# Optimization experiments

Measured on AMD Instinct MI355X. Metric: run time of the kernel, lower is better.

The kernel has to match this reference:

```python
import jax, jax.numpy as jnp
import numpy as np
from jax import lax

EPS = 1e-5
DW_TH = 4.0   # threshold in cut_conv3_5_DW
PW_TH = 1e-3  # threshold in cut_conv3_5_PW


def _bn(x, gamma, beta, mean, var):
    # inference-mode batchnorm over channel dim (NCHW)
    scale = (gamma * lax.rsqrt(var + EPS))[None, :, None, None]
    shift = (beta - mean * gamma * lax.rsqrt(var + EPS))[None, :, None, None]
    return x * scale + shift


def _channel_cut(x, th):
    # faithful to max(torch.max(x[m][k]), -torch.min(x[m][k])) == max |x| per (n, c)
    max_obs = jnp.max(jnp.abs(x), axis=(2, 3), keepdims=True)  # [N, C, 1, 1]
    return jnp.where(max_obs < th, jnp.zeros_like(x), x)


def setup_inputs() -> dict:
    key = jax.random.key(0)
    ks = jax.random.split(key, 6)
    N, Cin, Cout, H, W = 32, 256, 512, 56, 56
    x = jax.random.normal(ks[0], (N, Cin, H, W), dtype=jnp.float32)
    dw_w = jax.random.normal(ks[1], (Cin, 1, 3, 3), dtype=jnp.float32) * 0.3
    dw_b = jax.random.normal(ks[2], (Cin,), dtype=jnp.float32) * 0.1
    pw_w = jax.random.normal(ks[3], (Cout, Cin), dtype=jnp.float32) * 0.05
    pw_b = jax.random.normal(ks[4], (Cout,), dtype=jnp.float32) * 0.1
    return {
        "x": x,
        "dw_w": dw_w,
        "dw_b": dw_b,
        "bn1_gamma": jnp.ones((Cin,), jnp.float32) * 2.0,
        "bn1_beta": jnp.zeros((Cin,), jnp.float32),
        "bn1_mean": jnp.zeros((Cin,), jnp.float32),
        "bn1_var": jnp.ones((Cin,), jnp.float32),
        "pw_w": pw_w,
        "pw_b": pw_b,
        "bn2_gamma": jnp.ones((Cout,), jnp.float32),
        "bn2_beta": jnp.zeros((Cout,), jnp.float32),
        "bn2_mean": jnp.zeros((Cout,), jnp.float32),
        "bn2_var": jnp.ones((Cout,), jnp.float32),
    }


def reference(x, dw_w, dw_b, bn1_gamma, bn1_beta, bn1_mean, bn1_var,
              pw_w, pw_b, bn2_gamma, bn2_beta, bn2_mean, bn2_var):
    Cin = x.shape[1]
    # depthwise 3x3 conv, padding=1 (groups == in_channels)
    y = lax.conv_general_dilated(
        x, dw_w, window_strides=(1, 1), padding=((1, 1), (1, 1)),
        dimension_numbers=("NCHW", "OIHW", "NCHW"),
        feature_group_count=Cin,
    ) + dw_b[None, :, None, None]
    y = jax.nn.relu(_bn(y, bn1_gamma, bn1_beta, bn1_mean, bn1_var))
    y = _channel_cut(y, DW_TH)
    # pointwise 1x1 conv as channel GEMM
    z = jnp.einsum("oc,nchw->nohw", pw_w, y) + pw_b[None, :, None, None]
    z = jax.nn.relu(_bn(z, bn2_gamma, bn2_beta, bn2_mean, bn2_var))
    z = _channel_cut(z, PW_TH)
    return z
```

## Files before the change

kernel.cpp:

```cpp
#include <hip/hip_runtime.h>
#include <hip/hip_bf16.h>

#define HW 3136
#define CIN 256
#define COUT 512
#define NBATCH 32
#define EPS 1e-5f
#define DW_TH 4.0f
#define PW_TH 1e-3f

#define DPITCH 564

typedef __attribute__((ext_vector_type(8))) short s16x8;
typedef __attribute__((ext_vector_type(4))) float f32x4;
typedef unsigned int u32;
typedef unsigned short u16;

__device__ __forceinline__ void async_copy16(void* lds, const void* g) {
    __builtin_amdgcn_global_load_lds((const __attribute__((address_space(1))) unsigned int*)g,
                                     (__attribute__((address_space(3))) unsigned int*)lds,
                                     16, 0, 0);
}

__device__ __forceinline__ u16 bf16_bits(float f) {
    __hip_bfloat16 h = __float2bfloat16(f);
    union { __hip_bfloat16 h; u16 u; } cv; cv.h = h; return cv.u;
}

__global__ __launch_bounds__(256) void dw_kernel(
    const float* __restrict__ x, const float* __restrict__ dww, const float* __restrict__ dwb,
    const float* __restrict__ g1, const float* __restrict__ b1,
    const float* __restrict__ m1, const float* __restrict__ v1,
    const float* __restrict__ pww, const float* __restrict__ pwb,
    const float* __restrict__ g2, const float* __restrict__ b2,
    const float* __restrict__ m2, const float* __restrict__ v2,
    u16* __restrict__ y, float* __restrict__ dwmaxp,
    u16* __restrict__ wb, float2* __restrict__ scsh)
{
    const int bid = blockIdx.x;
    const int t = threadIdx.x;

    if (bid >= 1792) {
        const int gid = (bid - 1792) * 256 + t;
        const int base = gid * 8;
        const float4 a = *(const float4*)(pww + base);
        const float4 b = *(const float4*)(pww + base + 4);
        union { u16 u[8]; s16x8 v; } pk;
        pk.u[0] = bf16_bits(a.x); pk.u[1] = bf16_bits(a.y);
        pk.u[2] = bf16_bits(a.z); pk.u[3] = bf16_bits(a.w);
        pk.u[4] = bf16_bits(b.x); pk.u[5] = bf16_bits(b.y);
        pk.u[6] = bf16_bits(b.z); pk.u[7] = bf16_bits(b.w);
        *(s16x8*)(wb + base) = pk.v;
        if (gid < COUT) {
            const float sc = g2[gid] * rsqrtf(v2[gid] + EPS);
            const float sh = fmaf(-m2[gid], sc, b2[gid]) + pwb[gid] * sc;
            scsh[gid] = make_float2(sc, sh);
        }
        return;
    }

    __shared__ float xs[32 * DPITCH];
    __shared__ float sm[256];

    const int n   = bid / 56;
    const int rem = bid % 56;
    const int hs  = rem >> 3;
    const int cg  = rem & 7;

    const int g0     = hs * 8 - 1;
    const int gstart = (g0 < 0) ? 0 : g0;
    const int nrows  = (hs == 0 || hs == 6) ? 9 : 10;
    const int dst0   = (hs == 0) ? 1 : 0;
    const int cnt4   = nrows * 14;

    if (hs == 0) {
        for (int i = t; i < 32 * 14; i += 256) {
            const int c = i / 14, j = i - c * 14;
            *(float4*)&xs[c * DPITCH + j * 4] = make_float4(0.f, 0.f, 0.f, 0.f);
        }
    } else if (hs == 6) {
        for (int i = t; i < 32 * 14; i += 256) {
            const int c = i / 14, j = i - c * 14;
            *(float4*)&xs[c * DPITCH + 9 * 56 + j * 4] = make_float4(0.f, 0.f, 0.f, 0.f);
        }
    }

    {
        const float* gbase = x + (size_t)(n * CIN + cg * 32) * HW + gstart * 56;
        const int w = t >> 6, lane = t & 63;
        for (int i = 0; i < 24; ++i) {
            const int j = w + 4 * i;
            const int c = j / 3, s = j - c * 3;
            const int i4 = s * 64 + lane;
            if (i4 < cnt4)
                async_copy16(&xs[c * DPITCH + dst0 * 56 + i4 * 4],
                             gbase + (size_t)c * HW + i4 * 4);
        }
    }
    __syncthreads();

    const int r = t >> 5;
    const int c = t & 31;
    float vmax = 0.f;
    {
        const int ch = cg * 32 + c;
        const float* wp = dww + ch * 9;
        const float w00 = wp[0], w01 = wp[1], w02 = wp[2];
        const float w10 = wp[3], w11 = wp[4], w12 = wp[5];
        const float w20 = wp[6], w21 = wp[7], w22 = wp[8];
        const float sc = g1[ch] * rsqrtf(v1[ch] + EPS);
        const float sh = fmaf(-m1[ch], sc, b1[ch]) + dwb[ch] * sc;

        const float* rm = &xs[c * DPITCH + r * 56];
        const float* r0 = rm + 56;
        const float* rp = rm + 112;
        const int grow = hs * 8 + r;
        u16* yo = y + (size_t)(n * HW + grow * 56) * CIN + ch;

        float4 cm = *(const float4*)rm;
        float4 c0 = *(const float4*)r0;
        float4 cp = *(const float4*)rp;
        float lm = 0.f, l0 = 0.f, lp = 0.f;

        for (int chk = 0; chk < 14; ++chk) {
            float4 nm, n0, np;
            if (chk < 13) {
                nm = *(const float4*)(rm + 4 * chk + 4);
                n0 = *(const float4*)(r0 + 4 * chk + 4);
                np = *(const float4*)(rp + 4 * chk + 4);
            } else {
                nm = n0 = np = make_float4(0.f, 0.f, 0.f, 0.f);
            }
            float s0 = w00*lm   + w01*cm.x + w02*cm.y
                     + w10*l0   + w11*c0.x + w12*c0.y
                     + w20*lp   + w21*cp.x + w22*cp.y;
            float s1 = w00*cm.x + w01*cm.y + w02*cm.z
                     + w10*c0.x + w11*c0.y + w12*c0.z
                     + w20*cp.x + w21*cp.y + w22*cp.z;
            float s2 = w00*cm.y + w01*cm.z + w02*cm.w
                     + w10*c0.y + w11*c0.z + w12*c0.w
                     + w20*cp.y + w21*cp.z + w22*cp.w;
            float s3 = w00*cm.z + w01*cm.w + w02*nm.x
                     + w10*c0.z + w11*c0.w + w12*n0.x
                     + w20*cp.z + w21*cp.w + w22*np.x;
            const float v0  = fmaxf(fmaf(s0, sc, sh), 0.f);
            const float v1s = fmaxf(fmaf(s1, sc, sh), 0.f);
            const float v2s = fmaxf(fmaf(s2, sc, sh), 0.f);
            const float v3  = fmaxf(fmaf(s3, sc, sh), 0.f);
            vmax = fmaxf(fmaxf(vmax, fmaxf(v0, v1s)), fmaxf(v2s, v3));
            yo[(4 * chk + 0) * CIN] = bf16_bits(v0);
            yo[(4 * chk + 1) * CIN] = bf16_bits(v1s);
            yo[(4 * chk + 2) * CIN] = bf16_bits(v2s);
            yo[(4 * chk + 3) * CIN] = bf16_bits(v3);
            lm = cm.w; l0 = c0.w; lp = cp.w;
            cm = nm; c0 = n0; cp = np;
        }
    }

    sm[t] = vmax;
    __syncthreads();
    if (t < 32) {
        float m = sm[t];
#pragma unroll
        for (int k = 1; k < 8; ++k) m = fmaxf(m, sm[t + 32 * k]);
        dwmaxp[(n * 7 + hs) * 256 + cg * 32 + t] = m;
    }
}

__global__ __launch_bounds__(256, 2) void pw_kernel(
    const u16* __restrict__ y, const u16* __restrict__ wb,
    const float2* __restrict__ scsh, const float* __restrict__ dwmaxp,
    float* __restrict__ out, float* __restrict__ omaxp)
{
    __shared__ __align__(16) u16 Wt[3][256 * 32];
    __shared__ __align__(16) u16 Yt[3][128 * 32];
    __shared__ __align__(16) u16 msk[CIN];

    const int bid = blockIdx.x;
    const int g   = (bid & 7) * 224 + (bid >> 3);
    const int ot  = g & 1;
    const int r2  = g >> 1;
    const int hwt = r2 % 28;
    const int n   = r2 / 28;

    const int t = threadIdx.x;
    const int w = t >> 6;
    const int l = t & 63;
    const int lo = l & 15, hi = l >> 4;

    const int o_blk  = ot * 256;
    const int hw_blk = n * HW + hwt * 112;

    const u16* wg = wb + (size_t)(o_blk + w * 64 + (l >> 2)) * CIN + (l & 3) * 8;
    const u16* yg = y  + (size_t)(hw_blk + (l >> 2)) * CIN + (l & 3) * 8;

    {
        float mm = dwmaxp[n * 7 * 256 + t];
#pragma unroll
        for (int s2 = 1; s2 < 7; ++s2) mm = fmaxf(mm, dwmaxp[(n * 7 + s2) * 256 + t]);
        msk[t] = (mm >= DW_TH) ? (u16)0xFFFFu : (u16)0u;
    }
    __syncthreads();

    f32x4 acc[4][7];
#pragma unroll
    for (int s = 0; s < 4; ++s)
#pragma unroll
        for (int j = 0; j < 7; ++j) acc[s][j] = (f32x4){0.f, 0.f, 0.f, 0.f};

#define STAGE(buf, k0) do {                                                            \
        char* WtB_ = (char*)&Wt[buf][0];                                               \
        char* YtB_ = (char*)&Yt[buf][0];                                               \
        _Pragma("unroll")                                                              \
        for (int i_ = 0; i_ < 4; ++i_)                                                 \
            async_copy16(WtB_ + (w * 64 + i_ * 16) * 64 + l * 16,                      \
                         wg + (k0) + (size_t)(i_ * 16) * CIN);                         \
        const int j0_ = 2 * w;                                                         \
        async_copy16(YtB_ + (j0_ * 16) * 64 + l * 16,                                  \
                     yg + (k0) + (size_t)(j0_ * 16) * CIN);                            \
        const int j1_ = j0_ + 1, sj_ = (j1_ == 7) ? 6 : j1_;                           \
        async_copy16(YtB_ + (j1_ * 16) * 64 + l * 16,                                  \
                     yg + (k0) + (size_t)(sj_ * 16) * CIN);                            \
    } while (0)

    STAGE(0, 0);
    asm volatile("" ::: "memory");
    STAGE(1, 32);

#pragma unroll
    for (int tk = 0; tk < 8; ++tk) {
        const int cur = tk % 3;
        if (tk < 7) asm volatile("s_waitcnt vmcnt(6)" ::: "memory");
        else        asm volatile("s_waitcnt vmcnt(0)" ::: "memory");
        __builtin_amdgcn_s_barrier();
        __builtin_amdgcn_sched_barrier(0);
        if (tk < 6) { STAGE((tk + 2) % 3, (tk + 2) * 32); }

        const char* WtB = (const char*)&Wt[cur][0];
        const char* YtB = (const char*)&Yt[cur][0];
        const s16x8 m8 = *(const s16x8*)((const char*)msk + tk * 64 + hi * 16);

        s16x8 af[4], bf7[7];
#pragma unroll
        for (int s = 0; s < 4; ++s) {
            af[s] = *(const s16x8*)(WtB + (w * 64 + s * 16 + lo) * 64 + hi * 16);
            af[s] = af[s] & m8;
        }
#pragma unroll
        for (int j = 0; j < 7; ++j)
            bf7[j] = *(const s16x8*)(YtB + (j * 16 + lo) * 64 + hi * 16);

        __builtin_amdgcn_s_setprio(1);
#pragma unroll
        for (int s = 0; s < 4; ++s)
#pragma unroll
            for (int j = 0; j < 7; ++j)
                acc[s][j] = __builtin_amdgcn_mfma_f32_16x16x32_bf16(af[s], bf7[j], acc[s][j], 0, 0, 0);
        __builtin_amdgcn_s_setprio(0);
    }
#undef STAGE

#pragma unroll
    for (int s = 0; s < 4; ++s) {
#pragma unroll
        for (int r = 0; r < 4; ++r) {
            const int o = o_blk + w * 64 + s * 16 + hi * 4 + r;
            const float2 ss = scsh[o];
            float m = 0.f;
            float* op = out + (size_t)(n * COUT + o) * HW + hwt * 112 + lo;
#pragma unroll
            for (int j = 0; j < 7; ++j) {
                const float v = fmaxf(fmaf(acc[s][j][r], ss.x, ss.y), 0.f);
                op[j * 16] = v;
                m = fmaxf(m, v);
            }
            m = fmaxf(m, __shfl_xor(m, 1));
            m = fmaxf(m, __shfl_xor(m, 2));
            m = fmaxf(m, __shfl_xor(m, 4));
            m = fmaxf(m, __shfl_xor(m, 8));
            if (lo == 0) omaxp[(size_t)(n * COUT + o) * 28 + hwt] = m;
        }
    }
}

__global__ __launch_bounds__(64) void pwcut_kernel(const float* __restrict__ omaxp, float* __restrict__ out)
{
    const int b = blockIdx.x;
    const int t = threadIdx.x;
    float m = (t < 28) ? omaxp[(size_t)b * 28 + t] : 0.f;
#pragma unroll
    for (int d = 1; d < 64; d <<= 1) m = fmaxf(m, __shfl_xor(m, d));
    if (m >= PW_TH) return;
    float4* p = (float4*)(out + (size_t)b * HW);
    const float4 z = make_float4(0.f, 0.f, 0.f, 0.f);
    for (int i = t; i < HW / 4; i += 64) p[i] = z;
}

extern "C" void kernel_launch(void* const* d_in, const int* in_sizes, int n_in,
                              void* d_out, int out_size, void* d_ws, size_t ws_size,
                              hipStream_t stream) {
    const float* x   = (const float*)d_in[0];
    const float* dww = (const float*)d_in[1];
    const float* dwb = (const float*)d_in[2];
    const float* g1  = (const float*)d_in[3];
    const float* b1  = (const float*)d_in[4];
    const float* m1  = (const float*)d_in[5];
    const float* v1  = (const float*)d_in[6];
    const float* pww = (const float*)d_in[7];
    const float* pwb = (const float*)d_in[8];
    const float* g2  = (const float*)d_in[9];
    const float* b2  = (const float*)d_in[10];
    const float* m2  = (const float*)d_in[11];
    const float* v2  = (const float*)d_in[12];
    float* out = (float*)d_out;

    float*  omaxp  = (float*)d_ws;
    float*  dwmaxp = (float*)((char*)d_ws + (2 << 20));
    float2* scsh   = (float2*)((char*)d_ws + (3 << 20));
    u16*    wbf    = (u16*)((char*)d_ws + (4 << 20));
    u16*    yv     = (u16*)((char*)d_ws + (8 << 20));

    dw_kernel<<<1792 + 64, 256, 0, stream>>>(x, dww, dwb, g1, b1, m1, v1,
                                             pww, pwb, g2, b2, m2, v2,
                                             yv, dwmaxp, wbf, scsh);
    pw_kernel<<<1792, 256, 0, stream>>>(yv, wbf, scsh, dwmaxp, out, omaxp);
    pwcut_kernel<<<NBATCH * COUT, 64, 0, stream>>>(omaxp, out);
}
```

Measured before the change: 368.8 us.

## Fuse pointwise channel-cut into GEMM via atomics and halve output tile

Removes the separate pwcut kernel: per-channel max is accumulated with atomicMax into a global buffer, and the last block finishing each (batch, 128-channel) group, detected with an atomic counter, zeroes the channels below threshold. The GEMM tile shrinks from 256 to 128 output channels, doubling the grid and raising occupancy to 3 blocks per CU, with less LDS and fewer registers per block. This saves a kernel launch and a full read of the partial maxima. In exchange it adds atomics, a threadfence, and a serial zeroing loop run by the last block, and each block now reuses every loaded Y tile across half as many output channels.

After: 832.1 us. +125.6%, slower.

```diff
diff --git a/kernel.cpp b/kernel.cpp
--- a/kernel.cpp
+++ b/kernel.cpp
@@ -35,7 +35,8 @@
     const float* __restrict__ g2, const float* __restrict__ b2,
     const float* __restrict__ m2, const float* __restrict__ v2,
     u16* __restrict__ y, float* __restrict__ dwmaxp,
-    u16* __restrict__ wb, float2* __restrict__ scsh)
+    u16* __restrict__ wb, float2* __restrict__ scsh,
+    u32* __restrict__ omax, u32* __restrict__ cnt)
 {
     const int bid = blockIdx.x;
     const int t = threadIdx.x;
@@ -51,6 +52,8 @@
         pk.u[4] = bf16_bits(b.x); pk.u[5] = bf16_bits(b.y);
         pk.u[6] = bf16_bits(b.z); pk.u[7] = bf16_bits(b.w);
         *(s16x8*)(wb + base) = pk.v;
+        omax[gid] = 0u;
+        if (gid < 128) cnt[gid] = 0u;
         if (gid < COUT) {
             const float sc = g2[gid] * rsqrtf(v2[gid] + EPS);
             const float sh = fmaf(-m2[gid], sc, b2[gid]) + pwb[gid] * sc;
@@ -167,19 +170,20 @@
     }
 }
 
-__global__ __launch_bounds__(256, 2) void pw_kernel(
+__global__ __launch_bounds__(256, 3) void pw_kernel(
     const u16* __restrict__ y, const u16* __restrict__ wb,
     const float2* __restrict__ scsh, const float* __restrict__ dwmaxp,
-    float* __restrict__ out, float* __restrict__ omaxp)
+    float* __restrict__ out, u32* __restrict__ omax, u32* __restrict__ cnt)
 {
-    __shared__ __align__(16) u16 Wt[3][256 * 32];
+    __shared__ __align__(16) u16 Wt[3][128 * 32];
     __shared__ __align__(16) u16 Yt[3][128 * 32];
     __shared__ __align__(16) u16 msk[CIN];
+    __shared__ u32 scnt;
 
     const int bid = blockIdx.x;
-    const int g   = (bid & 7) * 224 + (bid >> 3);
-    const int ot  = g & 1;
-    const int r2  = g >> 1;
+    const int g   = (bid & 7) * 448 + (bid >> 3);
+    const int ot  = g & 3;
+    const int r2  = g >> 2;
     const int hwt = r2 % 28;
     const int n   = r2 / 28;
 
@@ -188,10 +192,10 @@
     const int l = t & 63;
     const int lo = l & 15, hi = l >> 4;
 
-    const int o_blk  = ot * 256;
+    const int o_blk  = ot * 128;
     const int hw_blk = n * HW + hwt * 112;
 
-    const u16* wg = wb + (size_t)(o_blk + w * 64 + (l >> 2)) * CIN + (l & 3) * 8;
+    const u16* wg = wb + (size_t)(o_blk + w * 32 + (l >> 2)) * CIN + (l & 3) * 8;
     const u16* yg = y  + (size_t)(hw_blk + (l >> 2)) * CIN + (l & 3) * 8;
 
     {
@@ -202,9 +206,9 @@
     }
     __syncthreads();
 
-    f32x4 acc[4][7];
-#pragma unroll
-    for (int s = 0; s < 4; ++s)
+    f32x4 acc[2][7];
+#pragma unroll
+    for (int s = 0; s < 2; ++s)
 #pragma unroll
         for (int j = 0; j < 7; ++j) acc[s][j] = (f32x4){0.f, 0.f, 0.f, 0.f};
 
@@ -212,15 +216,16 @@
         char* WtB_ = (char*)&Wt[buf][0];                                               \
         char* YtB_ = (char*)&Yt[buf][0];                                               \
         _Pragma("unroll")                                                              \
-        for (int i_ = 0; i_ < 4; ++i_)                                                 \
-            async_copy16(WtB_ + (w * 64 + i_ * 16) * 64 + l * 16,                      \
+        for (int i_ = 0; i_ < 2; ++i_)                                                 \
+            async_copy16(WtB_ + (w * 32 + i_ * 16) * 64 + l * 16,                      \
                          wg + (k0) + (size_t)(i_ * 16) * CIN);                         \
-        const int j0_ = 2 * w;                                                         \
-        async_copy16(YtB_ + (j0_ * 16) * 64 + l * 16,                                  \
-                     yg + (k0) + (size_t)(j0_ * 16) * CIN);                            \
-        const int j1_ = j0_ + 1, sj_ = (j1_ == 7) ? 6 : j1_;                           \
-        async_copy16(YtB_ + (j1_ * 16) * 64 + l * 16,                                  \
-                     yg + (k0) + (size_t)(sj_ * 16) * CIN);                            \
+        _Pragma("unroll")                                                              \
+        for (int i_ = 0; i_ < 2; ++i_) {                                               \
+            const int j_ = w + 4 * i_;                                                 \
+            const int sj_ = (j_ == 7) ? 6 : j_;                                        \
+            async_copy16(YtB_ + (j_ * 16) * 64 + l * 16,                               \
+                         yg + (k0) + (size_t)(sj_ * 16) * CIN);                        \
+        }                                                                              \
     } while (0)
 
     STAGE(0, 0);
@@ -230,7 +235,7 @@
 #pragma unroll
     for (int tk = 0; tk < 8; ++tk) {
         const int cur = tk % 3;
-        if (tk < 7) asm volatile("s_waitcnt vmcnt(6)" ::: "memory");
+        if (tk < 7) asm volatile("s_waitcnt vmcnt(4)" ::: "memory");
         else        asm volatile("s_waitcnt vmcnt(0)" ::: "memory");
         __builtin_amdgcn_s_barrier();
         __builtin_amdgcn_sched_barrier(0);
@@ -240,10 +245,10 @@
         const char* YtB = (const char*)&Yt[cur][0];
         const s16x8 m8 = *(const s16x8*)((const char*)msk + tk * 64 + hi * 16);
 
-        s16x8 af[4], bf7[7];
-#pragma unroll
-        for (int s = 0; s < 4; ++s) {
-            af[s] = *(const s16x8*)(WtB + (w * 64 + s * 16 + lo) * 64 + hi * 16);
+        s16x8 af[2], bf7[7];
+#pragma unroll
+        for (int s = 0; s < 2; ++s) {
+            af[s] = *(const s16x8*)(WtB + (w * 32 + s * 16 + lo) * 64 + hi * 16);
             af[s] = af[s] & m8;
         }
 #pragma unroll
@@ -252,7 +257,7 @@
 
         __builtin_amdgcn_s_setprio(1);
 #pragma unroll
-        for (int s = 0; s < 4; ++s)
+        for (int s = 0; s < 2; ++s)
 #pragma unroll
             for (int j = 0; j < 7; ++j)
                 acc[s][j] = __builtin_amdgcn_mfma_f32_16x16x32_bf16(af[s], bf7[j], acc[s][j], 0, 0, 0);
@@ -261,10 +266,10 @@
 #undef STAGE
 
 #pragma unroll
-    for (int s = 0; s < 4; ++s) {
+    for (int s = 0; s < 2; ++s) {
 #pragma unroll
         for (int r = 0; r < 4; ++r) {
-            const int o = o_blk + w * 64 + s * 16 + hi * 4 + r;
+            const int o = o_blk + w * 32 + s * 16 + hi * 4 + r;
             const float2 ss = scsh[o];
             float m = 0.f;
             float* op = out + (size_t)(n * COUT + o) * HW + hwt * 112 + lo;
@@ -278,22 +283,22 @@
             m = fmaxf(m, __shfl_xor(m, 2));
             m = fmaxf(m, __shfl_xor(m, 4));
             m = fmaxf(m, __shfl_xor(m, 8));
-            if (lo == 0) omaxp[(size_t)(n * COUT + o) * 28 + hwt] = m;
-        }
-    }
-}
-
-__global__ __launch_bounds__(64) void pwcut_kernel(const float* __restrict__ omaxp, float* __restrict__ out)
-{
-    const int b = blockIdx.x;
-    const int t = threadIdx.x;
-    float m = (t < 28) ? omaxp[(size_t)b * 28 + t] : 0.f;
-#pragma unroll
-    for (int d = 1; d < 64; d <<= 1) m = fmaxf(m, __shfl_xor(m, d));
-    if (m >= PW_TH) return;
-    float4* p = (float4*)(out + (size_t)b * HW);
-    const float4 z = make_float4(0.f, 0.f, 0.f, 0.f);
-    for (int i = t; i < HW / 4; i += 64) p[i] = z;
+            if (lo == 0) atomicMax(&omax[n * COUT + o], __float_as_uint(m));
+        }
+    }
+
+    __threadfence();
+    if (t == 0) scnt = atomicAdd(&cnt[n * 4 + ot], 1u);
+    __syncthreads();
+    if (scnt == 27u) {
+        const int c = t >> 1, hf = t & 1;
+        const u32 mo = atomicMax(&omax[n * COUT + o_blk + c], 0u);
+        if (__uint_as_float(mo) < PW_TH) {
+            float4* p = (float4*)(out + (size_t)(n * COUT + o_blk + c) * HW) + hf * 392;
+            const float4 z = make_float4(0.f, 0.f, 0.f, 0.f);
+            for (int i = 0; i < 392; ++i) p[i] = z;
+        }
+    }
 }
 
 extern "C" void kernel_launch(void* const* d_in, const int* in_sizes, int n_in,
@@ -314,7 +319,8 @@
     const float* v2  = (const float*)d_in[12];
     float* out = (float*)d_out;
 
-    float*  omaxp  = (float*)d_ws;
+    u32*    omax   = (u32*)d_ws;
+    u32*    cnt    = (u32*)((char*)d_ws + (64 << 10));
     float*  dwmaxp = (float*)((char*)d_ws + (2 << 20));
     float2* scsh   = (float2*)((char*)d_ws + (3 << 20));
     u16*    wbf    = (u16*)((char*)d_ws + (4 << 20));
@@ -322,7 +328,6 @@
 
     dw_kernel<<<1792 + 64, 256, 0, stream>>>(x, dww, dwb, g1, b1, m1, v1,
                                              pww, pwb, g2, b2, m2, v2,
-                                             yv, dwmaxp, wbf, scsh);
-    pw_kernel<<<1792, 256, 0, stream>>>(yv, wbf, scsh, dwmaxp, out, omaxp);
-    pwcut_kernel<<<NBATCH * COUT, 64, 0, stream>>>(omaxp, out);
-}
+                                             yv, dwmaxp, wbf, scsh, omax, cnt);
+    pw_kernel<<<3584, 256, 0, stream>>>(yv, wbf, scsh, dwmaxp, out, omax, cnt);
+}
```

## Split depthwise blocks to 16 channels with half-row threads; swizzle pointwise LDS tiles

Applied to the files above, without the earlier changes.

The depthwise kernel now uses blocks of 16 channels instead of 32, doubling the grid. Each thread handles half a row (28 pixels) rather than a full row, which halves the LDS tile and the per-thread serial work and should raise occupancy and latency hiding. Separately, the pointwise GEMM applies an XOR swizzle to the 16-byte column chunk used for global-to-LDS staging and for fragment reads, to reduce LDS bank conflicts. Costs include more blocks with duplicated halo rows and narrower bf16 store runs per block.

After: 377.4 us. 2.3% more time.

```diff
diff --git a/kernel.cpp b/kernel.cpp
--- a/kernel.cpp
+++ b/kernel.cpp
@@ -40,8 +40,8 @@
     const int bid = blockIdx.x;
     const int t = threadIdx.x;
 
-    if (bid >= 1792) {
-        const int gid = (bid - 1792) * 256 + t;
+    if (bid >= 3584) {
+        const int gid = (bid - 3584) * 256 + t;
         const int base = gid * 8;
         const float4 a = *(const float4*)(pww + base);
         const float4 b = *(const float4*)(pww + base + 4);
@@ -59,13 +59,13 @@
         return;
     }
 
-    __shared__ float xs[32 * DPITCH];
+    __shared__ float xs[16 * DPITCH];
     __shared__ float sm[256];
 
-    const int n   = bid / 56;
-    const int rem = bid % 56;
-    const int hs  = rem >> 3;
-    const int cg  = rem & 7;
+    const int n   = bid / 112;
+    const int rem = bid % 112;
+    const int hs  = rem >> 4;
+    const int cq  = rem & 15;
 
     const int g0     = hs * 8 - 1;
     const int gstart = (g0 < 0) ? 0 : g0;
@@ -74,21 +74,21 @@
     const int cnt4   = nrows * 14;
 
     if (hs == 0) {
-        for (int i = t; i < 32 * 14; i += 256) {
-            const int c = i / 14, j = i - c * 14;
+        if (t < 224) {
+            const int c = t / 14, j = t - c * 14;
             *(float4*)&xs[c * DPITCH + j * 4] = make_float4(0.f, 0.f, 0.f, 0.f);
         }
     } else if (hs == 6) {
-        for (int i = t; i < 32 * 14; i += 256) {
-            const int c = i / 14, j = i - c * 14;
+        if (t < 224) {
+            const int c = t / 14, j = t - c * 14;
             *(float4*)&xs[c * DPITCH + 9 * 56 + j * 4] = make_float4(0.f, 0.f, 0.f, 0.f);
         }
     }
 
     {
-        const float* gbase = x + (size_t)(n * CIN + cg * 32) * HW + gstart * 56;
+        const float* gbase = x + (size_t)(n * CIN + cq * 16) * HW + gstart * 56;
         const int w = t >> 6, lane = t & 63;
-        for (int i = 0; i < 24; ++i) {
+        for (int i = 0; i < 12; ++i) {
             const int j = w + 4 * i;
             const int c = j / 3, s = j - c * 3;
             const int i4 = s * 64 + lane;
@@ -99,11 +99,12 @@
     }
     __syncthreads();
 
-    const int r = t >> 5;
-    const int c = t & 31;
+    const int c  = t & 15;
+    const int r  = (t >> 4) & 7;
+    const int hf = t >> 7;
     float vmax = 0.f;
     {
-        const int ch = cg * 32 + c;
+        const int ch = cq * 16 + c;
         const float* wp = dww + ch * 9;
         const float w00 = wp[0], w01 = wp[1], w02 = wp[2];
         const float w10 = wp[3], w11 = wp[4], w12 = wp[5];
@@ -111,20 +112,22 @@
         const float sc = g1[ch] * rsqrtf(v1[ch] + EPS);
         const float sh = fmaf(-m1[ch], sc, b1[ch]) + dwb[ch] * sc;
 
-        const float* rm = &xs[c * DPITCH + r * 56];
+        const float* rm = &xs[c * DPITCH + r * 56 + hf * 28];
         const float* r0 = rm + 56;
         const float* rp = rm + 112;
         const int grow = hs * 8 + r;
-        u16* yo = y + (size_t)(n * HW + grow * 56) * CIN + ch;
+        u16* yo = y + (size_t)(n * HW + grow * 56 + hf * 28) * CIN + ch;
 
         float4 cm = *(const float4*)rm;
         float4 c0 = *(const float4*)r0;
         float4 cp = *(const float4*)rp;
-        float lm = 0.f, l0 = 0.f, lp = 0.f;
-
-        for (int chk = 0; chk < 14; ++chk) {
+        float lm, l0, lp;
+        if (hf) { lm = rm[-1]; l0 = r0[-1]; lp = rp[-1]; }
+        else    { lm = 0.f;   l0 = 0.f;   lp = 0.f; }
+
+        for (int chk = 0; chk < 7; ++chk) {
             float4 nm, n0, np;
-            if (chk < 13) {
+            if (!hf || chk < 6) {
                 nm = *(const float4*)(rm + 4 * chk + 4);
                 n0 = *(const float4*)(r0 + 4 * chk + 4);
                 np = *(const float4*)(rp + 4 * chk + 4);
@@ -159,11 +162,11 @@
 
     sm[t] = vmax;
     __syncthreads();
-    if (t < 32) {
+    if (t < 16) {
         float m = sm[t];
 #pragma unroll
-        for (int k = 1; k < 8; ++k) m = fmaxf(m, sm[t + 32 * k]);
-        dwmaxp[(n * 7 + hs) * 256 + cg * 32 + t] = m;
+        for (int k = 1; k < 16; ++k) m = fmaxf(m, sm[t + 16 * k]);
+        dwmaxp[(n * 7 + hs) * 256 + cq * 16 + t] = m;
     }
 }
 
@@ -191,8 +194,9 @@
     const int o_blk  = ot * 256;
     const int hw_blk = n * HW + hwt * 112;
 
-    const u16* wg = wb + (size_t)(o_blk + w * 64 + (l >> 2)) * CIN + (l & 3) * 8;
-    const u16* yg = y  + (size_t)(hw_blk + (l >> 2)) * CIN + (l & 3) * 8;
+    const int sl = ((l & 3) ^ ((l >> 2) & 3)) * 8;
+    const u16* wg = wb + (size_t)(o_blk + w * 64 + (l >> 2)) * CIN + sl;
+    const u16* yg = y  + (size_t)(hw_blk + (l >> 2)) * CIN + sl;
 
     {
         float mm = dwmaxp[n * 7 * 256 + t];
@@ -239,16 +243,17 @@
         const char* WtB = (const char*)&Wt[cur][0];
         const char* YtB = (const char*)&Yt[cur][0];
         const s16x8 m8 = *(const s16x8*)((const char*)msk + tk * 64 + hi * 16);
+        const int sx = (hi ^ (lo & 3)) * 16;
 
         s16x8 af[4], bf7[7];
 #pragma unroll
         for (int s = 0; s < 4; ++s) {
-            af[s] = *(const s16x8*)(WtB + (w * 64 + s * 16 + lo) * 64 + hi * 16);
+            af[s] = *(const s16x8*)(WtB + (w * 64 + s * 16 + lo) * 64 + sx);
             af[s] = af[s] & m8;
         }
 #pragma unroll
         for (int j = 0; j < 7; ++j)
-            bf7[j] = *(const s16x8*)(YtB + (j * 16 + lo) * 64 + hi * 16);
+            bf7[j] = *(const s16x8*)(YtB + (j * 16 + lo) * 64 + sx);
 
         __builtin_amdgcn_s_setprio(1);
 #pragma unroll
@@ -320,7 +325,7 @@
     u16*    wbf    = (u16*)((char*)d_ws + (4 << 20));
     u16*    yv     = (u16*)((char*)d_ws + (8 << 20));
 
-    dw_kernel<<<1792 + 64, 256, 0, stream>>>(x, dww, dwb, g1, b1, m1, v1,
+    dw_kernel<<<3584 + 64, 256, 0, stream>>>(x, dww, dwb, g1, b1, m1, v1,
                                              pww, pwb, g2, b2, m2, v2,
                                              yv, dwmaxp, wbf, scsh);
     pw_kernel<<<1792, 256, 0, stream>>>(yv, wbf, scsh, dwmaxp, out, omaxp);
```

## Drop LDS staging in depthwise kernel; map one thread per row per channel

Applied to the files above, without the earlier changes.

The depthwise kernel no longer stages input tiles in shared memory with async copies. Each block now covers 4 channels across all 56 rows of one image, and each thread reads its three input rows directly from global memory. Border handling is folded into the weights by zeroing them at the edges. The per-channel max becomes a single reduction per image, so the pointwise kernel's 7-way partial max combine goes away. This trades the LDS staging and its barrier for redundant global row reads (each row is loaded by three threads) and leaves 32 of 256 threads idle. The y stores are also now scattered across only 4 channels per block, which may hurt write coalescing.

Measured after the change: 568.6 us. +54.2%, slower.

```diff
diff --git a/kernel.cpp b/kernel.cpp
--- a/kernel.cpp
+++ b/kernel.cpp
@@ -8,8 +8,6 @@
 #define EPS 1e-5f
 #define DW_TH 4.0f
 #define PW_TH 1e-3f
-
-#define DPITCH 564
 
 typedef __attribute__((ext_vector_type(8))) short s16x8;
 typedef __attribute__((ext_vector_type(4))) float f32x4;
@@ -40,8 +38,8 @@
     const int bid = blockIdx.x;
     const int t = threadIdx.x;
 
-    if (bid >= 1792) {
-        const int gid = (bid - 1792) * 256 + t;
+    if (bid >= 2048) {
+        const int gid = (bid - 2048) * 256 + t;
         const int base = gid * 8;
         const float4 a = *(const float4*)(pww + base);
         const float4 b = *(const float4*)(pww + base + 4);
@@ -59,69 +57,39 @@
         return;
     }
 
-    __shared__ float xs[32 * DPITCH];
     __shared__ float sm[256];
 
-    const int n   = bid / 56;
-    const int rem = bid % 56;
-    const int hs  = rem >> 3;
-    const int cg  = rem & 7;
-
-    const int g0     = hs * 8 - 1;
-    const int gstart = (g0 < 0) ? 0 : g0;
-    const int nrows  = (hs == 0 || hs == 6) ? 9 : 10;
-    const int dst0   = (hs == 0) ? 1 : 0;
-    const int cnt4   = nrows * 14;
-
-    if (hs == 0) {
-        for (int i = t; i < 32 * 14; i += 256) {
-            const int c = i / 14, j = i - c * 14;
-            *(float4*)&xs[c * DPITCH + j * 4] = make_float4(0.f, 0.f, 0.f, 0.f);
-        }
-    } else if (hs == 6) {
-        for (int i = t; i < 32 * 14; i += 256) {
-            const int c = i / 14, j = i - c * 14;
-            *(float4*)&xs[c * DPITCH + 9 * 56 + j * 4] = make_float4(0.f, 0.f, 0.f, 0.f);
-        }
-    }
-
-    {
-        const float* gbase = x + (size_t)(n * CIN + cg * 32) * HW + gstart * 56;
-        const int w = t >> 6, lane = t & 63;
-        for (int i = 0; i < 24; ++i) {
-            const int j = w + 4 * i;
-            const int c = j / 3, s = j - c * 3;
-            const int i4 = s * 64 + lane;
-            if (i4 < cnt4)
-                async_copy16(&xs[c * DPITCH + dst0 * 56 + i4 * 4],
-                             gbase + (size_t)c * HW + i4 * 4);
-        }
-    }
-    __syncthreads();
-
-    const int r = t >> 5;
-    const int c = t & 31;
+    const int n  = bid >> 6;
+    const int cq = bid & 63;
+    const int c4 = t / 56;
+    const int r  = t - c4 * 56;
+    const bool active = (c4 < 4);
+
     float vmax = 0.f;
-    {
-        const int ch = cg * 32 + c;
+    if (active) {
+        const int ch = cq * 4 + c4;
         const float* wp = dww + ch * 9;
-        const float w00 = wp[0], w01 = wp[1], w02 = wp[2];
-        const float w10 = wp[3], w11 = wp[4], w12 = wp[5];
-        const float w20 = wp[6], w21 = wp[7], w22 = wp[8];
+        const float km = (r > 0) ? 1.f : 0.f;
+        const float kp = (r < 55) ? 1.f : 0.f;
+        const float w00 = wp[0] * km, w01 = wp[1] * km, w02 = wp[2] * km;
+        const float w10 = wp[3],      w11 = wp[4],      w12 = wp[5];
+        const float w20 = wp[6] * kp, w21 = wp[7] * kp, w22 = wp[8] * kp;
         const float sc = g1[ch] * rsqrtf(v1[ch] + EPS);
         const float sh = fmaf(-m1[ch], sc, b1[ch]) + dwb[ch] * sc;
 
-        const float* rm = &xs[c * DPITCH + r * 56];
-        const float* r0 = rm + 56;
-        const float* rp = rm + 112;
-        const int grow = hs * 8 + r;
-        u16* yo = y + (size_t)(n * HW + grow * 56) * CIN + ch;
+        const float* xb = x + (size_t)(n * CIN + ch) * HW;
+        const float* rm = xb + (size_t)((r == 0)  ? 0  : r - 1) * 56;
+        const float* r0 = xb + (size_t)r * 56;
+        const float* rp = xb + (size_t)((r == 55) ? 55 : r + 1) * 56;
+
+        u16* yo = y + (size_t)(n * HW + r * 56) * CIN + ch;
 
         float4 cm = *(const float4*)rm;
         float4 c0 = *(const float4*)r0;
         float4 cp = *(const float4*)rp;
         float lm = 0.f, l0 = 0.f, lp = 0.f;
 
+#pragma unroll
         for (int chk = 0; chk < 14; ++chk) {
             float4 nm, n0, np;
             if (chk < 13) {
@@ -159,11 +127,11 @@
 
     sm[t] = vmax;
     __syncthreads();
-    if (t < 32) {
-        float m = sm[t];
-#pragma unroll
-        for (int k = 1; k < 8; ++k) m = fmaxf(m, sm[t + 32 * k]);
-        dwmaxp[(n * 7 + hs) * 256 + cg * 32 + t] = m;
+    if (t < 4) {
+        float m = sm[t * 56];
+#pragma unroll
+        for (int k = 1; k < 56; ++k) m = fmaxf(m, sm[t * 56 + k]);
+        dwmaxp[n * CIN + cq * 4 + t] = m;
     }
 }
 
@@ -194,12 +162,7 @@
     const u16* wg = wb + (size_t)(o_blk + w * 64 + (l >> 2)) * CIN + (l & 3) * 8;
     const u16* yg = y  + (size_t)(hw_blk + (l >> 2)) * CIN + (l & 3) * 8;
 
-    {
-        float mm = dwmaxp[n * 7 * 256 + t];
-#pragma unroll
-        for (int s2 = 1; s2 < 7; ++s2) mm = fmaxf(mm, dwmaxp[(n * 7 + s2) * 256 + t]);
-        msk[t] = (mm >= DW_TH) ? (u16)0xFFFFu : (u16)0u;
-    }
+    msk[t] = (dwmaxp[n * CIN + t] >= DW_TH) ? (u16)0xFFFFu : (u16)0u;
     __syncthreads();
 
     f32x4 acc[4][7];
@@ -320,7 +283,7 @@
     u16*    wbf    = (u16*)((char*)d_ws + (4 << 20));
     u16*    yv     = (u16*)((char*)d_ws + (8 << 20));
 
-    dw_kernel<<<1792 + 64, 256, 0, stream>>>(x, dww, dwb, g1, b1, m1, v1,
+    dw_kernel<<<2048 + 64, 256, 0, stream>>>(x, dww, dwb, g1, b1, m1, v1,
                                              pww, pwb, g2, b2, m2, v2,
                                              yv, dwmaxp, wbf, scsh);
     pw_kernel<<<1792, 256, 0, stream>>>(yv, wbf, scsh, dwmaxp, out, omaxp);
```
